# Kernel optimization log

Measured on AMD Instinct MI355X. Metric: run time of the kernel, lower is better.

Reference implementation:

```python
import jax, jax.numpy as jnp
import numpy as np

N = 100000   # nodes
E = 1600000  # edges
IN = 256
H = 128


def gcn_conv(x, W, b, src, dst, n):
    """PyG GCNConv (eval): self-loops + symmetric normalization + linear + scatter-add."""
    h = x @ W                                   # [n, out]
    loop = jnp.arange(n)
    s = jnp.concatenate([src, loop])            # [E+n]
    d = jnp.concatenate([dst, loop])
    deg = jax.ops.segment_sum(jnp.ones_like(d, dtype=h.dtype), d, num_segments=n)
    dinv = jnp.where(deg > 0, jax.lax.rsqrt(deg), 0.0)
    norm = dinv[s] * dinv[d]                    # [E+n]
    out = jax.ops.segment_sum(h[s] * norm[:, None], d, num_segments=n)
    return out + b


def setup_inputs() -> dict:
    key = jax.random.key(0)
    ks = jax.random.split(key, 8)
    x = jax.random.normal(ks[0], (N, IN), dtype=jnp.float32)
    edge_index = jax.random.randint(ks[1], (2, E), 0, N, dtype=jnp.int64)
    W1 = jax.random.normal(ks[2], (IN, H), dtype=jnp.float32) * (1.0 / np.sqrt(IN))
    b1 = jnp.zeros((H,), dtype=jnp.float32)
    W2 = jax.random.normal(ks[3], (H, H), dtype=jnp.float32) * (1.0 / np.sqrt(H))
    b2 = jnp.zeros((H,), dtype=jnp.float32)
    W3 = jax.random.normal(ks[4], (H, H), dtype=jnp.float32) * (1.0 / np.sqrt(H))
    b3 = jnp.zeros((H,), dtype=jnp.float32)
    return {"x": x, "edge_index": edge_index, "W1": W1, "b1": b1,
            "W2": W2, "b2": b2, "W3": W3, "b3": b3}


def reference(x, edge_index, W1, b1, W2, b2, W3, b3):
    src, dst = edge_index[0], edge_index[1]
    n = x.shape[0]
    h = gcn_conv(x, W1, b1, src, dst, n)
    h = jax.nn.relu(h)                          # dropout inactive in eval
    h = gcn_conv(h, W2, b2, src, dst, n)
    h = jax.nn.relu(h)
    h = gcn_conv(h, W3, b3, src, dst, n)
    return h
```

## Files before the change

### kernel.cpp

```cpp
#include <hip/hip_runtime.h>

#define HDIM 128

typedef unsigned int uint;
typedef unsigned short ushort;
typedef __attribute__((ext_vector_type(8))) short short8;
typedef __attribute__((ext_vector_type(4))) float f32x4;

typedef __attribute__((address_space(3))) uint  lds_u32_t;
typedef const __attribute__((address_space(1))) uint g_u32_t;
#define GLDS16(gp, lp) __builtin_amdgcn_global_load_lds((g_u32_t*)(gp), (lds_u32_t*)(lp), 16, 0, 0)

__device__ inline ushort f2bf(float f) {
    uint u = __float_as_uint(f);
    uint rounding = 0x7fffu + ((u >> 16) & 1u);
    return (ushort)((u + rounding) >> 16);
}
__device__ inline float bf2f(ushort h) { return __uint_as_float(((uint)h) << 16); }

__device__ inline float4 bf4_to_f4(uint2 u) {
    float4 r;
    r.x = __uint_as_float(u.x << 16);
    r.y = __uint_as_float(u.x & 0xffff0000u);
    r.z = __uint_as_float(u.y << 16);
    r.w = __uint_as_float(u.y & 0xffff0000u);
    return r;
}


__global__ __launch_bounds__(256) void k_count(const int* __restrict__ dst,
                                               int* __restrict__ cnt,
                                               int* __restrict__ rank, int e) {
    int i = blockIdx.x * 256 + threadIdx.x;
    if (i < e) rank[i] = atomicAdd(&cnt[dst[i]], 1);
}

__global__ __launch_bounds__(256) void k_dinv(const int* __restrict__ cnt,
                                              float* __restrict__ dinv, int n) {
    int i = blockIdx.x * 256 + threadIdx.x;
    if (i < n) dinv[i] = rsqrtf((float)(cnt[i] + 1));
}

__global__ __launch_bounds__(256) void k_scan1(const int* __restrict__ cnt,
                                               int* __restrict__ offs,
                                               int* __restrict__ bsum, int n) {
    __shared__ int sm[256];
    int tid = threadIdx.x;
    int i = blockIdx.x * 256 + tid;
    int v = (i < n) ? cnt[i] : 0;
    sm[tid] = v;
    __syncthreads();
    for (int off = 1; off < 256; off <<= 1) {
        int t = (tid >= off) ? sm[tid - off] : 0;
        __syncthreads();
        sm[tid] += t;
        __syncthreads();
    }
    if (i < n) offs[i] = sm[tid] - v;
    if (tid == 255) bsum[blockIdx.x] = sm[255];
}

__global__ __launch_bounds__(512) void k_scan2(int* __restrict__ bsum, int nb) {
    __shared__ int sm[512];
    int tid = threadIdx.x;
    int v = (tid < nb) ? bsum[tid] : 0;
    sm[tid] = v;
    __syncthreads();
    for (int off = 1; off < 512; off <<= 1) {
        int t = (tid >= off) ? sm[tid - off] : 0;
        __syncthreads();
        sm[tid] += t;
        __syncthreads();
    }
    if (tid < nb) bsum[tid] = sm[tid] - v;
}

__global__ __launch_bounds__(256) void k_scan3(int* __restrict__ offs,
                                               const int* __restrict__ bsum,
                                               int n, int e) {
    int i = blockIdx.x * 256 + threadIdx.x;
    if (i < n) offs[i] += bsum[blockIdx.x];
    if (i == 0) offs[n] = e;
}

__global__ __launch_bounds__(256) void k_fill(const int* __restrict__ src,
                                              const int* __restrict__ dst,
                                              const int* __restrict__ offs,
                                              const int* __restrict__ rank,
                                              int* __restrict__ csr, int e) {
    int i = blockIdx.x * 256 + threadIdx.x;
    if (i < e) {
        csr[offs[dst[i]] + rank[i]] = src[i];
    }
}


__global__ __launch_bounds__(256) void k_prep_w(const float* __restrict__ W,
                                                ushort* __restrict__ wt_hi,
                                                ushort* __restrict__ wt_lo, int K) {
    int idx = blockIdx.x * 256 + threadIdx.x;
    if (idx < K * HDIM) {
        int k = idx >> 7;
        int c = idx & 127;
        float v = W[idx];
        ushort h = f2bf(v);
        ushort l = f2bf(v - bf2f(h));
        int kt = k >> 5, kk = k & 31;
        int pos = kt * 4096 + c * 32 + (kk ^ (((c >> 1) & 3) << 3));
        wt_hi[pos] = h;
        wt_lo[pos] = l;
    }
}


template<int K, bool XF32>
__global__ __launch_bounds__(512, XF32 ? 2 : 4)
void k_mm(const float* __restrict__ Xf,
          const ushort* __restrict__ XH,
          const ushort* __restrict__ XL,
          const ushort* __restrict__ WH,
          const ushort* __restrict__ WL,
          const float* __restrict__ dinv,
          ushort* __restrict__ g, int n)
{
    constexpr int NKT = K / 32;
    __shared__ ushort lds[2][NKT][128][32];

    const int tid  = threadIdx.x;
    const int wv   = tid >> 6;
    const int lane = tid & 63;
    const int r    = lane & 15;
    const int gq   = lane >> 4;
    const int sw   = (r >> 1) & 3;

    {
        const ushort* plane = (tid < 256) ? WH : WL;
        ushort* dstp = (tid < 256) ? &lds[0][0][0][0] : &lds[1][0][0][0];
        int t = tid & 255;
        constexpr int CH = (NKT * 4096) / (256 * 8);
        #pragma unroll
        for (int i = 0; i < CH; i++) {
            int off = (i * 256 + t) * 8;
            GLDS16(plane + off, dstp + off);
        }
    }

    const int tile = blockIdx.x * 8 + wv;
    const int ntiles = (n + 15) / 16;
    const bool active = tile < ntiles;
    const int row0 = active ? tile * 16 : 0;
    int rowr = row0 + r; if (rowr >= n) rowr = n - 1;

    f32x4 acc[8];
    #pragma unroll
    for (int m = 0; m < 8; m++) acc[m] = (f32x4){0.f, 0.f, 0.f, 0.f};

    if constexpr (!XF32) {
        short8 xh8[NKT], xl8[NKT];
        const size_t n32 = (size_t)n * 32;
        const size_t rowoff = (size_t)rowr * 32 + (size_t)(gq ^ sw) * 8;
        #pragma unroll
        for (int kt = 0; kt < NKT; kt++) {
            xh8[kt] = *(const short8*)(XH + (size_t)kt * n32 + rowoff);
            xl8[kt] = *(const short8*)(XL + (size_t)kt * n32 + rowoff);
        }
        __syncthreads();

        #pragma unroll
        for (int kt = 0; kt < NKT; kt++) {
            #pragma unroll
            for (int m = 0; m < 8; m++) {
                short8 ah = *(const short8*)&lds[0][kt][m * 16 + r][(gq ^ sw) * 8];
                short8 al = *(const short8*)&lds[1][kt][m * 16 + r][(gq ^ sw) * 8];
                acc[m] = __builtin_amdgcn_mfma_f32_16x16x32_bf16(ah, xh8[kt], acc[m], 0, 0, 0);
                acc[m] = __builtin_amdgcn_mfma_f32_16x16x32_bf16(ah, xl8[kt], acc[m], 0, 0, 0);
                acc[m] = __builtin_amdgcn_mfma_f32_16x16x32_bf16(al, xh8[kt], acc[m], 0, 0, 0);
            }
        }
    } else {
        float4 xf[2 * NKT];
        const float4* xp = (const float4*)(Xf + (size_t)rowr * K);
        #pragma unroll
        for (int kt = 0; kt < NKT; kt++) {
            xf[kt * 2]     = xp[kt * 8 + gq * 2];
            xf[kt * 2 + 1] = xp[kt * 8 + gq * 2 + 1];
        }
        __syncthreads();

        #pragma unroll
        for (int kt = 0; kt < NKT; kt++) {
            float v[8] = {xf[kt*2].x, xf[kt*2].y, xf[kt*2].z, xf[kt*2].w,
                          xf[kt*2+1].x, xf[kt*2+1].y, xf[kt*2+1].z, xf[kt*2+1].w};
            short8 bh, bl;
            #pragma unroll
            for (int q = 0; q < 8; q++) {
                ushort h = f2bf(v[q]);
                bh[q] = (short)h;
                bl[q] = (short)f2bf(v[q] - bf2f(h));
            }
            #pragma unroll
            for (int m = 0; m < 8; m++) {
                short8 ah = *(const short8*)&lds[0][kt][m * 16 + r][(gq ^ sw) * 8];
                short8 al = *(const short8*)&lds[1][kt][m * 16 + r][(gq ^ sw) * 8];
                acc[m] = __builtin_amdgcn_mfma_f32_16x16x32_bf16(ah, bh, acc[m], 0, 0, 0);
                acc[m] = __builtin_amdgcn_mfma_f32_16x16x32_bf16(ah, bl, acc[m], 0, 0, 0);
                acc[m] = __builtin_amdgcn_mfma_f32_16x16x32_bf16(al, bh, acc[m], 0, 0, 0);
            }
        }
    }

    int row = row0 + r;
    if (active && row < n) {
        float di = dinv[row];
        #pragma unroll
        for (int m = 0; m < 8; m++) {
            int wcol = m * 16 + gq * 4;
            f32x4 a = acc[m];
            uint2 pk;
            pk.x = (uint)f2bf(a[0] * di) | ((uint)f2bf(a[1] * di) << 16);
            pk.y = (uint)f2bf(a[2] * di) | ((uint)f2bf(a[3] * di) << 16);
            *(uint2*)(g + (size_t)row * HDIM + wcol) = pk;
        }
    }
}


template<bool RELU, bool EMIT_SPLIT>
__global__ __launch_bounds__(256) void k_gather(const ushort* __restrict__ g,
                                                const int* __restrict__ csr,
                                                const int* __restrict__ offs,
                                                const float* __restrict__ dinv,
                                                const float* __restrict__ bias,
                                                float* __restrict__ out,
                                                ushort* __restrict__ ah,
                                                ushort* __restrict__ al, int n)
{
    int t    = blockIdx.x * 256 + threadIdx.x;
    int node = t >> 5;
    int l    = t & 31;
    if (node >= n) return;

    int e0 = offs[node];
    int e1 = offs[node + 1];

    float4 acc = bf4_to_f4(*(const uint2*)(g + (size_t)node * HDIM + l * 4));

    int e = e0;
    for (; e + 4 <= e1; e += 4) {
        int s0 = csr[e], s1 = csr[e + 1], s2 = csr[e + 2], s3 = csr[e + 3];
        float4 v0 = bf4_to_f4(*(const uint2*)(g + (size_t)s0 * HDIM + l * 4));
        float4 v1 = bf4_to_f4(*(const uint2*)(g + (size_t)s1 * HDIM + l * 4));
        float4 v2 = bf4_to_f4(*(const uint2*)(g + (size_t)s2 * HDIM + l * 4));
        float4 v3 = bf4_to_f4(*(const uint2*)(g + (size_t)s3 * HDIM + l * 4));
        acc.x += v0.x + v1.x + v2.x + v3.x;
        acc.y += v0.y + v1.y + v2.y + v3.y;
        acc.z += v0.z + v1.z + v2.z + v3.z;
        acc.w += v0.w + v1.w + v2.w + v3.w;
    }
    for (; e < e1; e++) {
        int s = csr[e];
        float4 v = bf4_to_f4(*(const uint2*)(g + (size_t)s * HDIM + l * 4));
        acc.x += v.x; acc.y += v.y; acc.z += v.z; acc.w += v.w;
    }

    float di  = dinv[node];
    float4 bb = *(const float4*)(bias + l * 4);
    float4 o;
    o.x = fmaf(di, acc.x, bb.x);
    o.y = fmaf(di, acc.y, bb.y);
    o.z = fmaf(di, acc.z, bb.z);
    o.w = fmaf(di, acc.w, bb.w);
    if (RELU) {
        o.x = fmaxf(o.x, 0.f); o.y = fmaxf(o.y, 0.f);
        o.z = fmaxf(o.z, 0.f); o.w = fmaxf(o.w, 0.f);
    }
    if (EMIT_SPLIT) {
        ushort h0 = f2bf(o.x), h1 = f2bf(o.y), h2 = f2bf(o.z), h3 = f2bf(o.w);
        uint2 ph, pl;
        ph.x = (uint)h0 | ((uint)h1 << 16);
        ph.y = (uint)h2 | ((uint)h3 << 16);
        pl.x = (uint)f2bf(o.x - bf2f(h0)) | ((uint)f2bf(o.y - bf2f(h1)) << 16);
        pl.y = (uint)f2bf(o.z - bf2f(h2)) | ((uint)f2bf(o.w - bf2f(h3)) << 16);
        int kt = l >> 3;
        size_t base = (size_t)kt * n * 32 + (size_t)node * 32
                    + (((l & 7) * 4) ^ (((node >> 1) & 3) << 3));
        *(uint2*)(ah + base) = ph;
        *(uint2*)(al + base) = pl;
    } else {
        *(float4*)(out + (size_t)node * HDIM + l * 4) = o;
    }
}


extern "C" void kernel_launch(void* const* d_in, const int* in_sizes, int n_in,
                              void* d_out, int out_size, void* d_ws, size_t ws_size,
                              hipStream_t stream)
{
    const float* x  = (const float*)d_in[0];
    const int*   ei = (const int*)d_in[1];
    const float* W1 = (const float*)d_in[2];
    const float* b1 = (const float*)d_in[3];
    const float* W2 = (const float*)d_in[4];
    const float* b2 = (const float*)d_in[5];
    const float* W3 = (const float*)d_in[6];
    const float* b3 = (const float*)d_in[7];
    float* out = (float*)d_out;

    const int n = in_sizes[0] / 256;
    const int E = in_sizes[1] / 2;
    const int* src = ei;
    const int* dst = ei + E;

    char*   ws   = (char*)d_ws;
    float*  dinv = (float*)(ws);
    int*    cnt  = (int*)(ws + (512 << 10));
    int*    offs = (int*)(ws + (1 << 20));
    int*    bsum = (int*)(ws + 1536 * 1024);
    int*    csr  = (int*)(ws + 1600 * 1024);
    int*    rank = (int*)(ws + (size_t)(8 << 20));
    ushort* wh   = (ushort*)(ws + 14848 * 1024);
    ushort* wl   = (ushort*)(ws + 15104 * 1024);
    ushort* g    = (ushort*)(ws + (size_t)(16 << 20));
    ushort* xh2  = (ushort*)(ws + (size_t)(42 << 20));
    ushort* xl2  = (ushort*)(ws + (size_t)(68 << 20));

    dim3 blk(256);
    int ngrid = (n + 255) / 256;
    int egrid = (E + 255) / 256;

    hipMemsetAsync(cnt, 0, (size_t)n * 4, stream);
    k_count<<<egrid, blk, 0, stream>>>(dst, cnt, rank, E);
    k_dinv<<<ngrid, blk, 0, stream>>>(cnt, dinv, n);
    k_scan1<<<ngrid, blk, 0, stream>>>(cnt, offs, bsum, n);
    k_scan2<<<1, 512, 0, stream>>>(bsum, ngrid);
    k_scan3<<<ngrid, blk, 0, stream>>>(offs, bsum, n, E);
    k_fill<<<egrid, blk, 0, stream>>>(src, dst, offs, rank, csr, E);

    int ntiles  = (n + 15) / 16;
    int mm_grid = (ntiles + 7) / 8;
    int gat_grid = (int)(((size_t)n * 32 + 255) / 256);

    k_prep_w<<<(256 * HDIM + 255) / 256, blk, 0, stream>>>(W1, wh, wl, 256);
    k_mm<256, true><<<mm_grid, 512, 0, stream>>>(x, nullptr, nullptr, wh, wl, dinv, g, n);
    k_gather<true, true><<<gat_grid, blk, 0, stream>>>(g, csr, offs, dinv, b1, nullptr, xh2, xl2, n);
    k_prep_w<<<(128 * HDIM + 255) / 256, blk, 0, stream>>>(W2, wh, wl, 128);
    k_mm<128, false><<<mm_grid, 512, 0, stream>>>(nullptr, xh2, xl2, wh, wl, dinv, g, n);
    k_gather<true, true><<<gat_grid, blk, 0, stream>>>(g, csr, offs, dinv, b2, nullptr, xh2, xl2, n);
    k_prep_w<<<(128 * HDIM + 255) / 256, blk, 0, stream>>>(W3, wh, wl, 128);
    k_mm<128, false><<<mm_grid, 512, 0, stream>>>(nullptr, xh2, xl2, wh, wl, dinv, g, n);
    k_gather<false, false><<<gat_grid, blk, 0, stream>>>(g, csr, offs, dinv, b3, out, nullptr, nullptr, n);
}
```

Baseline: 402.8 us.

## Drop bf16 hi/lo split to single bf16 GEMM with persistent prefetching tiles

Measured after the change: 453.4 us. 12.6% more time.

```diff
diff --git a/kernel.cpp b/kernel.cpp
--- a/kernel.cpp
+++ b/kernel.cpp
@@ -96,144 +96,130 @@
 
 
 __global__ __launch_bounds__(256) void k_prep_w(const float* __restrict__ W,
-                                                ushort* __restrict__ wt_hi,
-                                                ushort* __restrict__ wt_lo, int K) {
+                                                ushort* __restrict__ wt, int K) {
     int idx = blockIdx.x * 256 + threadIdx.x;
     if (idx < K * HDIM) {
         int k = idx >> 7;
         int c = idx & 127;
-        float v = W[idx];
-        ushort h = f2bf(v);
-        ushort l = f2bf(v - bf2f(h));
-        int kt = k >> 5, kk = k & 31;
-        int pos = kt * 4096 + c * 32 + (kk ^ (((c >> 1) & 3) << 3));
-        wt_hi[pos] = h;
-        wt_lo[pos] = l;
-    }
-}
-
-
-template<int K, bool XF32>
-__global__ __launch_bounds__(512, XF32 ? 2 : 4)
-void k_mm(const float* __restrict__ Xf,
-          const ushort* __restrict__ XH,
-          const ushort* __restrict__ XL,
-          const ushort* __restrict__ WH,
-          const ushort* __restrict__ WL,
+        int pos = (k >> 5) * 4096 + c * 32 + ((k & 31) ^ (((c >> 1) & 3) << 3));
+        wt[pos] = f2bf(W[idx]);
+    }
+}
+
+
+__global__ __launch_bounds__(256) void k_split_x(const float* __restrict__ X,
+                                                 ushort* __restrict__ XP, int n) {
+    int u  = blockIdx.x * 256 + threadIdx.x;
+    int kt = blockIdx.y;
+    if (u >= n * 4) return;
+    int node = u >> 2;
+    int p    = u & 3;
+    int lu   = p ^ ((node >> 1) & 3);
+    const float* xs = X + (size_t)node * 256 + kt * 32 + lu * 8;
+    float4 a = *(const float4*)xs;
+    float4 b = *(const float4*)(xs + 4);
+    uint2 pk;
+    pk.x = (uint)f2bf(a.x) | ((uint)f2bf(a.y) << 16);
+    pk.y = (uint)f2bf(a.z) | ((uint)f2bf(a.w) << 16);
+    uint2 pk2;
+    pk2.x = (uint)f2bf(b.x) | ((uint)f2bf(b.y) << 16);
+    pk2.y = (uint)f2bf(b.z) | ((uint)f2bf(b.w) << 16);
+    uint4 o = make_uint4(pk.x, pk.y, pk2.x, pk2.y);
+    *(uint4*)(XP + (size_t)kt * n * 32 + (size_t)node * 32 + p * 8) = o;
+}
+
+
+template<int NKT>
+__global__ __launch_bounds__(512, 2)
+void k_mm(const ushort* __restrict__ XP,
+          const ushort* __restrict__ WP,
           const float* __restrict__ dinv,
-          ushort* __restrict__ g, int n)
+          ushort* __restrict__ g, int n, int nblocks)
 {
-    constexpr int NKT = K / 32;
-    __shared__ ushort lds[2][NKT][128][32];
+    __shared__ ushort w[NKT][128][32];
 
     const int tid  = threadIdx.x;
     const int wv   = tid >> 6;
     const int lane = tid & 63;
     const int r    = lane & 15;
     const int gq   = lane >> 4;
-    const int sw   = (r >> 1) & 3;
+    const int pu8  = (gq ^ ((r >> 1) & 3)) * 8;
 
     {
-        const ushort* plane = (tid < 256) ? WH : WL;
-        ushort* dstp = (tid < 256) ? &lds[0][0][0][0] : &lds[1][0][0][0];
-        int t = tid & 255;
-        constexpr int CH = (NKT * 4096) / (256 * 8);
+        constexpr int CH = NKT * 4096 / (512 * 8);
         #pragma unroll
         for (int i = 0; i < CH; i++) {
-            int off = (i * 256 + t) * 8;
-            GLDS16(plane + off, dstp + off);
+            int off = (i * 512 + tid) * 8;
+            GLDS16(WP + off, ((ushort*)w) + off);
         }
     }
 
-    const int tile = blockIdx.x * 8 + wv;
     const int ntiles = (n + 15) / 16;
-    const bool active = tile < ntiles;
-    const int row0 = active ? tile * 16 : 0;
-    int rowr = row0 + r; if (rowr >= n) rowr = n - 1;
-
-    f32x4 acc[8];
-    #pragma unroll
-    for (int m = 0; m < 8; m++) acc[m] = (f32x4){0.f, 0.f, 0.f, 0.f};
-
-    if constexpr (!XF32) {
-        short8 xh8[NKT], xl8[NKT];
-        const size_t n32 = (size_t)n * 32;
-        const size_t rowoff = (size_t)rowr * 32 + (size_t)(gq ^ sw) * 8;
-        #pragma unroll
-        for (int kt = 0; kt < NKT; kt++) {
-            xh8[kt] = *(const short8*)(XH + (size_t)kt * n32 + rowoff);
-            xl8[kt] = *(const short8*)(XL + (size_t)kt * n32 + rowoff);
+    const size_t n32 = (size_t)n * 32;
+    const int tstep  = nblocks * 8;
+    int tile = blockIdx.x * 8 + wv;
+
+    short8 xc[NKT], xn[NKT];
+    if (tile < ntiles) {
+        int rowr = tile * 16 + r; if (rowr >= n) rowr = 0;
+        size_t ro = (size_t)rowr * 32 + pu8;
+        #pragma unroll
+        for (int kt = 0; kt < NKT; kt++)
+            xc[kt] = *(const short8*)(XP + kt * n32 + ro);
+    }
+
+    __syncthreads();
+
+    while (tile < ntiles) {
+        int tnext = tile + tstep;
+        if (tnext < ntiles) {
+            int rn = tnext * 16 + r; if (rn >= n) rn = 0;
+            size_t ro2 = (size_t)rn * 32 + pu8;
+            #pragma unroll
+            for (int kt = 0; kt < NKT; kt++)
+                xn[kt] = *(const short8*)(XP + kt * n32 + ro2);
         }
-        __syncthreads();
-
+
+        f32x4 acc[8];
+        #pragma unroll
+        for (int m = 0; m < 8; m++) acc[m] = (f32x4){0.f, 0.f, 0.f, 0.f};
         #pragma unroll
         for (int kt = 0; kt < NKT; kt++) {
             #pragma unroll
             for (int m = 0; m < 8; m++) {
-                short8 ah = *(const short8*)&lds[0][kt][m * 16 + r][(gq ^ sw) * 8];
-                short8 al = *(const short8*)&lds[1][kt][m * 16 + r][(gq ^ sw) * 8];
-                acc[m] = __builtin_amdgcn_mfma_f32_16x16x32_bf16(ah, xh8[kt], acc[m], 0, 0, 0);
-                acc[m] = __builtin_amdgcn_mfma_f32_16x16x32_bf16(ah, xl8[kt], acc[m], 0, 0, 0);
-                acc[m] = __builtin_amdgcn_mfma_f32_16x16x32_bf16(al, xh8[kt], acc[m], 0, 0, 0);
+                short8 ah = *(const short8*)&w[kt][m * 16 + r][pu8];
+                acc[m] = __builtin_amdgcn_mfma_f32_16x16x32_bf16(ah, xc[kt], acc[m], 0, 0, 0);
             }
         }
-    } else {
-        float4 xf[2 * NKT];
-        const float4* xp = (const float4*)(Xf + (size_t)rowr * K);
-        #pragma unroll
-        for (int kt = 0; kt < NKT; kt++) {
-            xf[kt * 2]     = xp[kt * 8 + gq * 2];
-            xf[kt * 2 + 1] = xp[kt * 8 + gq * 2 + 1];
-        }
-        __syncthreads();
-
-        #pragma unroll
-        for (int kt = 0; kt < NKT; kt++) {
-            float v[8] = {xf[kt*2].x, xf[kt*2].y, xf[kt*2].z, xf[kt*2].w,
-                          xf[kt*2+1].x, xf[kt*2+1].y, xf[kt*2+1].z, xf[kt*2+1].w};
-            short8 bh, bl;
-            #pragma unroll
-            for (int q = 0; q < 8; q++) {
-                ushort h = f2bf(v[q]);
-                bh[q] = (short)h;
-                bl[q] = (short)f2bf(v[q] - bf2f(h));
-            }
+
+        int row = tile * 16 + r;
+        if (row < n) {
+            float di = dinv[row];
             #pragma unroll
             for (int m = 0; m < 8; m++) {
-                short8 ah = *(const short8*)&lds[0][kt][m * 16 + r][(gq ^ sw) * 8];
-                short8 al = *(const short8*)&lds[1][kt][m * 16 + r][(gq ^ sw) * 8];
-                acc[m] = __builtin_amdgcn_mfma_f32_16x16x32_bf16(ah, bh, acc[m], 0, 0, 0);
-                acc[m] = __builtin_amdgcn_mfma_f32_16x16x32_bf16(ah, bl, acc[m], 0, 0, 0);
-                acc[m] = __builtin_amdgcn_mfma_f32_16x16x32_bf16(al, bh, acc[m], 0, 0, 0);
+                f32x4 a = acc[m];
+                uint2 pk;
+                pk.x = (uint)f2bf(a[0] * di) | ((uint)f2bf(a[1] * di) << 16);
+                pk.y = (uint)f2bf(a[2] * di) | ((uint)f2bf(a[3] * di) << 16);
+                *(uint2*)(g + (size_t)row * HDIM + m * 16 + gq * 4) = pk;
             }
         }
-    }
-
-    int row = row0 + r;
-    if (active && row < n) {
-        float di = dinv[row];
-        #pragma unroll
-        for (int m = 0; m < 8; m++) {
-            int wcol = m * 16 + gq * 4;
-            f32x4 a = acc[m];
-            uint2 pk;
-            pk.x = (uint)f2bf(a[0] * di) | ((uint)f2bf(a[1] * di) << 16);
-            pk.y = (uint)f2bf(a[2] * di) | ((uint)f2bf(a[3] * di) << 16);
-            *(uint2*)(g + (size_t)row * HDIM + wcol) = pk;
-        }
-    }
-}
-
-
-template<bool RELU, bool EMIT_SPLIT>
+
+        #pragma unroll
+        for (int kt = 0; kt < NKT; kt++) xc[kt] = xn[kt];
+        tile = tnext;
+    }
+}
+
+
+template<bool RELU, bool EMIT_PLANE>
 __global__ __launch_bounds__(256) void k_gather(const ushort* __restrict__ g,
                                                 const int* __restrict__ csr,
                                                 const int* __restrict__ offs,
                                                 const float* __restrict__ dinv,
                                                 const float* __restrict__ bias,
                                                 float* __restrict__ out,
-                                                ushort* __restrict__ ah,
-                                                ushort* __restrict__ al, int n)
+                                                ushort* __restrict__ ap, int n)
 {
     int t    = blockIdx.x * 256 + threadIdx.x;
     int node = t >> 5;
@@ -274,18 +260,14 @@
         o.x = fmaxf(o.x, 0.f); o.y = fmaxf(o.y, 0.f);
         o.z = fmaxf(o.z, 0.f); o.w = fmaxf(o.w, 0.f);
     }
-    if (EMIT_SPLIT) {
-        ushort h0 = f2bf(o.x), h1 = f2bf(o.y), h2 = f2bf(o.z), h3 = f2bf(o.w);
-        uint2 ph, pl;
-        ph.x = (uint)h0 | ((uint)h1 << 16);
-        ph.y = (uint)h2 | ((uint)h3 << 16);
-        pl.x = (uint)f2bf(o.x - bf2f(h0)) | ((uint)f2bf(o.y - bf2f(h1)) << 16);
-        pl.y = (uint)f2bf(o.z - bf2f(h2)) | ((uint)f2bf(o.w - bf2f(h3)) << 16);
+    if (EMIT_PLANE) {
+        uint2 ph;
+        ph.x = (uint)f2bf(o.x) | ((uint)f2bf(o.y) << 16);
+        ph.y = (uint)f2bf(o.z) | ((uint)f2bf(o.w) << 16);
         int kt = l >> 3;
         size_t base = (size_t)kt * n * 32 + (size_t)node * 32
                     + (((l & 7) * 4) ^ (((node >> 1) & 3) << 3));
-        *(uint2*)(ah + base) = ph;
-        *(uint2*)(al + base) = pl;
+        *(uint2*)(ap + base) = ph;
     } else {
         *(float4*)(out + (size_t)node * HDIM + l * 4) = o;
     }
@@ -318,11 +300,9 @@
     int*    bsum = (int*)(ws + 1536 * 1024);
     int*    csr  = (int*)(ws + 1600 * 1024);
     int*    rank = (int*)(ws + (size_t)(8 << 20));
-    ushort* wh   = (ushort*)(ws + 14848 * 1024);
-    ushort* wl   = (ushort*)(ws + 15104 * 1024);
+    ushort* wt   = (ushort*)(ws + 14848 * 1024);
     ushort* g    = (ushort*)(ws + (size_t)(16 << 20));
-    ushort* xh2  = (ushort*)(ws + (size_t)(42 << 20));
-    ushort* xl2  = (ushort*)(ws + (size_t)(68 << 20));
+    ushort* xp   = (ushort*)(ws + (size_t)(42 << 20));
 
     dim3 blk(256);
     int ngrid = (n + 255) / 256;
@@ -336,17 +316,21 @@
     k_scan3<<<ngrid, blk, 0, stream>>>(offs, bsum, n, E);
     k_fill<<<egrid, blk, 0, stream>>>(src, dst, offs, rank, csr, E);
 
-    int ntiles  = (n + 15) / 16;
-    int mm_grid = (ntiles + 7) / 8;
     int gat_grid = (int)(((size_t)n * 32 + 255) / 256);
-
-    k_prep_w<<<(256 * HDIM + 255) / 256, blk, 0, stream>>>(W1, wh, wl, 256);
-    k_mm<256, true><<<mm_grid, 512, 0, stream>>>(x, nullptr, nullptr, wh, wl, dinv, g, n);
-    k_gather<true, true><<<gat_grid, blk, 0, stream>>>(g, csr, offs, dinv, b1, nullptr, xh2, xl2, n);
-    k_prep_w<<<(128 * HDIM + 255) / 256, blk, 0, stream>>>(W2, wh, wl, 128);
-    k_mm<128, false><<<mm_grid, 512, 0, stream>>>(nullptr, xh2, xl2, wh, wl, dinv, g, n);
-    k_gather<true, true><<<gat_grid, blk, 0, stream>>>(g, csr, offs, dinv, b2, nullptr, xh2, xl2, n);
-    k_prep_w<<<(128 * HDIM + 255) / 256, blk, 0, stream>>>(W3, wh, wl, 128);
-    k_mm<128, false><<<mm_grid, 512, 0, stream>>>(nullptr, xh2, xl2, wh, wl, dinv, g, n);
-    k_gather<false, false><<<gat_grid, blk, 0, stream>>>(g, csr, offs, dinv, b3, out, nullptr, nullptr, n);
-}
+    const int MMB8 = 512;
+    const int MMB4 = 768;
+
+    k_prep_w<<<(256 * HDIM + 255) / 256, blk, 0, stream>>>(W1, wt, 256);
+    {
+        dim3 sg((n * 4 + 255) / 256, 8);
+        k_split_x<<<sg, blk, 0, stream>>>(x, xp, n);
+    }
+    k_mm<8><<<MMB8, 512, 0, stream>>>(xp, wt, dinv, g, n, MMB8);
+    k_gather<true, true><<<gat_grid, blk, 0, stream>>>(g, csr, offs, dinv, b1, nullptr, xp, n);
+    k_prep_w<<<(128 * HDIM + 255) / 256, blk, 0, stream>>>(W2, wt, 128);
+    k_mm<4><<<MMB4, 512, 0, stream>>>(xp, wt, dinv, g, n, MMB4);
+    k_gather<true, true><<<gat_grid, blk, 0, stream>>>(g, csr, offs, dinv, b2, nullptr, xp, n);
+    k_prep_w<<<(128 * HDIM + 255) / 256, blk, 0, stream>>>(W3, wt, 128);
+    k_mm<4><<<MMB4, 512, 0, stream>>>(xp, wt, dinv, g, n, MMB4);
+    k_gather<false, false><<<gat_grid, blk, 0, stream>>>(g, csr, offs, dinv, b3, out, nullptr, n);
+}
```
